# Kernel optimization log

Hardware: AMD Instinct MI355X
Metric: run time of the kernel (lower is better)

The kernel has to match this reference:

```python
import jax, jax.numpy as jnp
import numpy as np

DIM, H, W, B = 256, 64, 64, 2
N = H * W  # 4096 tokens (flattened feature map)
EPS = 1e-8


def setup_inputs() -> dict:
    key = jax.random.key(0)
    k0, k1, k2 = jax.random.split(key, 3)
    x = jax.random.normal(k0, (B, N, DIM), dtype=jnp.float32)
    y = jax.random.normal(k1, (B, N, DIM), dtype=jnp.float32)
    # orthogonal init of U (matches torch init.orthogonal_)
    U = jnp.linalg.qr(jax.random.normal(k2, (DIM, DIM), dtype=jnp.float32))[0]
    S1 = jnp.ones((DIM,), jnp.float32)
    S2 = jnp.ones((DIM,), jnp.float32)
    focus = jnp.float32(1.0)
    gating = jnp.float32(1.0)
    temp = jnp.float32(0.1)
    # abs_coords_y = arange(H).expand(W,-1).T.flatten() == floor(arange(N)/W)
    abs_y = jnp.floor_divide(jnp.arange(N, dtype=jnp.float32), jnp.float32(W))
    rel_coords_y = -abs_y[:, None] + abs_y[None, :]  # [N, N]
    return dict(x=x, y=y, U=U, S1=S1, S2=S2, focus=focus, gating=gating,
                temp=temp, rel_coords_y=rel_coords_y)


def reference(x, y, U, S1, S2, focus, gating, temp, rel_coords_y):
    Bb, Nn, d = x.shape
    # SpectralDecomp: x @ U^T @ diag(S^2) @ U, two branches stacked -> [B,2,N,d]
    xu = x @ U.T
    xs = jnp.stack([(xu * jnp.square(S1)) @ U, (xu * jnp.square(S2)) @ U], axis=1)
    # content score: [B,2,N,N]
    patch_score = jax.nn.softmax(
        jnp.einsum('bcnd,bmd->bcnm', xs, y) * (d ** -0.5), axis=-1)
    # position score: [N,N] broadcast to [B,2,N,N]
    pos_score = jax.nn.softmax(-jnp.abs(focus) * jnp.square(rel_coords_y), axis=-1)
    g = jax.nn.sigmoid(gating)
    attn = (1.0 - g) * patch_score + g * pos_score[None, None, :, :]
    attn = attn / attn.sum(axis=-1, keepdims=True)
    # entropy-based heat map + hard routing
    entropy = jnp.sum(-attn * jnp.log(attn + EPS), axis=-1).transpose(0, 2, 1)  # [B,N,2]
    hmap = 2.0 - 2.0 * jax.nn.sigmoid(temp * entropy)
    fgobg = hmap[..., 0] >= hmap[..., 1]  # [B,N]
    route = jnp.stack([fgobg, ~fgobg], axis=-1).astype(x.dtype)  # one-hot [B,N,2]
    heat_map = jnp.sum(hmap * route, axis=-1, keepdims=True)  # [B,N,1]
    # attend and select routed branch
    xo = jnp.einsum('bcnm,bmd->bncd', attn, y)  # [B,N,2,d]
    out = jnp.sum(xo * route[..., None], axis=-2)  # [B,N,d]
    return out, heat_map
```

## Files before the change

kernel.cpp:

```cpp
#include <hip/hip_runtime.h>
#include <math.h>

#define D      256
#define NTOK   4096
#define BATCH  2
#define NBC    4
#define NSPLIT 4
#define EPS    1e-8f
#define SCALE  0.0625f

typedef unsigned short ushortt;
typedef __attribute__((ext_vector_type(8))) short   bf16x8;
typedef __attribute__((ext_vector_type(4))) float   f32x4;
typedef __attribute__((ext_vector_type(4))) unsigned short u16x4;
typedef unsigned int u32;

__device__ __forceinline__ ushortt f2bf(float f) {
    u32 u = __builtin_bit_cast(u32, f);
    u += 0x7FFFu + ((u >> 16) & 1u);
    return (ushortt)(u >> 16);
}
__device__ __forceinline__ float bf2f(ushortt h) {
    u32 u = ((u32)h) << 16;
    return __builtin_bit_cast(float, u);
}

__device__ __forceinline__ void gload16(const ushortt* g, short* l) {
    __builtin_amdgcn_global_load_lds(
        (const __attribute__((address_space(1))) u32*)(const void*)g,
        (__attribute__((address_space(3))) u32*)(void*)l, 16, 0, 0);
}

__device__ __forceinline__ void mm_core(
    const ushortt* __restrict__ Ag, int lda,
    const ushortt* __restrict__ Bg, int ldb,
    int K, short* As, short* Bs, f32x4 acc[4][4])
{
    const int t = threadIdx.x, lane = t & 63, w = t >> 6;
    const int wr = w >> 1, wc = w & 1;
    const int l15 = lane & 15, l4 = lane >> 4;

    for (int k0 = 0; k0 < K; k0 += 64) {
        __syncthreads();
#pragma unroll
        for (int q = 0; q < 4; ++q) {
            int slot = (w * 4 + q) * 64 + lane;
            int r    = slot >> 3;
            int kgp  = slot & 7;
            int kg   = kgp ^ (r & 7);
            gload16(Ag + (size_t)r * lda + k0 + kg * 8, As + (w * 4 + q) * 512);
            gload16(Bg + (size_t)r * ldb + k0 + kg * 8, Bs + (w * 4 + q) * 512);
        }
        asm volatile("s_waitcnt vmcnt(0)" ::: "memory");
        __syncthreads();
#pragma unroll
        for (int kk = 0; kk < 2; ++kk) {
            bf16x8 af[4], bfr[4];
#pragma unroll
            for (int i = 0; i < 4; ++i) {
                int r  = wr * 64 + i * 16 + l15;
                int kg = kk * 4 + l4;
                af[i] = *(const bf16x8*)&As[(r * 8 + (kg ^ (r & 7))) * 8];
            }
#pragma unroll
            for (int j = 0; j < 4; ++j) {
                int c  = wc * 64 + j * 16 + l15;
                int kg = kk * 4 + l4;
                bfr[j] = *(const bf16x8*)&Bs[(c * 8 + (kg ^ (c & 7))) * 8];
            }
#pragma unroll
            for (int i = 0; i < 4; ++i)
#pragma unroll
                for (int j = 0; j < 4; ++j)
                    acc[i][j] = __builtin_amdgcn_mfma_f32_16x16x32_bf16(
                        af[i], bfr[j], acc[i][j], 0, 0, 0);
        }
    }
}

__global__ __launch_bounds__(256)
void k_prepM(const float* __restrict__ U, const float* __restrict__ S1,
             const float* __restrict__ S2, ushortt* __restrict__ M2b) {
    int idx = blockIdx.x * 256 + threadIdx.x;
    int c  = idx >> 16;
    int ij = idx & 65535;
    int i = ij >> 8, j = ij & 255;
    const float* S = c ? S2 : S1;
    float acc = 0.f;
    for (int k = 0; k < D; ++k) {
        float s = S[k];
        acc += U[k * D + i] * U[k * D + j] * (s * s);
    }
    M2b[idx] = f2bf(acc);
}

__global__ __launch_bounds__(256)
void k_cast(const float* __restrict__ x, const float* __restrict__ y,
            ushortt* __restrict__ xb, ushortt* __restrict__ yb) {
    int i = (blockIdx.x * 256 + threadIdx.x) * 4;
    float4 vx = *(const float4*)&x[i];
    float4 vy = *(const float4*)&y[i];
    u16x4 ox = { f2bf(vx.x), f2bf(vx.y), f2bf(vx.z), f2bf(vx.w) };
    u16x4 oy = { f2bf(vy.x), f2bf(vy.y), f2bf(vy.z), f2bf(vy.w) };
    *(u16x4*)&xb[i] = ox;
    *(u16x4*)&yb[i] = oy;
}

__global__ __launch_bounds__(256)
void k_transT(const float* __restrict__ y, ushortt* __restrict__ yT) {
    __shared__ float tile[64][65];
    const int b = blockIdx.z, d0 = blockIdx.y * 64, m0 = blockIdx.x * 64;
    const int t = threadIdx.x;
    const int c4 = (t & 15) * 4, r = t >> 4;
#pragma unroll
    for (int rr = r; rr < 64; rr += 16) {
        float4 v = *(const float4*)&y[((size_t)b * NTOK + m0 + rr) * D + d0 + c4];
        tile[rr][c4 + 0] = v.x; tile[rr][c4 + 1] = v.y;
        tile[rr][c4 + 2] = v.z; tile[rr][c4 + 3] = v.w;
    }
    __syncthreads();
    const int m4 = (t & 15) * 4;
#pragma unroll
    for (int dd = t >> 4; dd < 64; dd += 16) {
        u16x4 o = { f2bf(tile[m4 + 0][dd]), f2bf(tile[m4 + 1][dd]),
                    f2bf(tile[m4 + 2][dd]), f2bf(tile[m4 + 3][dd]) };
        *(u16x4*)&yT[((size_t)b * D + d0 + dd) * NTOK + m0 + m4] = o;
    }
}

__global__ __launch_bounds__(256)
void k_ysum(const float* __restrict__ y, float* __restrict__ Ysum) {
    const int blk = blockIdx.x;
    const int b = blk >> 6, ay = blk & 63;
    const int d = threadIdx.x;
    float acc = 0.f;
    const float* base = y + ((size_t)b * NTOK + ay * 64) * D + d;
#pragma unroll 8
    for (int w = 0; w < 64; ++w) acc += base[w * D];
    Ysum[(size_t)blk * D + d] = acc;
}

__global__ __launch_bounds__(256)
void k_posY(const float* __restrict__ Ysum, const float* __restrict__ focusp,
            float* __restrict__ posY) {
    __shared__ float e[64];
    const int blk = blockIdx.x;
    const int b = blk >> 6, ayq = blk & 63;
    const int t = threadIdx.x;
    const float f = fabsf(focusp[0]);
    if (t < 64) { float dy = (float)(t - ayq); e[t] = __expf(-f * dy * dy); }
    __syncthreads();
    float zs = 0.f;
#pragma unroll
    for (int j = 0; j < 64; ++j) zs += e[j];
    const float winv = 1.f / (64.f * zs);
    float acc = 0.f;
    const float* Yb = Ysum + (size_t)b * 64 * D + t;
#pragma unroll 8
    for (int aym = 0; aym < 64; ++aym) acc += e[aym] * Yb[aym * D];
    posY[(size_t)blk * D + t] = acc * winv;
}

__global__ __launch_bounds__(256)
void k_xs_mm(const ushortt* __restrict__ xb, const ushortt* __restrict__ M2b,
             ushortt* __restrict__ xsb) {
    __shared__ __align__(16) short As[8192];
    __shared__ __align__(16) short Bs[8192];
    const int bc = blockIdx.z, b = bc >> 1, c = bc & 1;
    const int d0 = blockIdx.x * 128, n0 = blockIdx.y * 128;
    f32x4 z = {0.f, 0.f, 0.f, 0.f};
    f32x4 acc[4][4];
#pragma unroll
    for (int i = 0; i < 4; ++i)
#pragma unroll
        for (int j = 0; j < 4; ++j) acc[i][j] = z;

    mm_core(xb + ((size_t)b * NTOK + n0) * D, D,
            M2b + (size_t)c * D * D + (size_t)d0 * D, D,
            D, As, Bs, acc);

    const int t = threadIdx.x, lane = t & 63, w = t >> 6;
    const int wr = w >> 1, wc = w & 1, l15 = lane & 15, l4 = lane >> 4;
#pragma unroll
    for (int i = 0; i < 4; ++i)
#pragma unroll
        for (int e = 0; e < 4; ++e) {
            int n = n0 + wr * 64 + i * 16 + l4 * 4 + e;
            ushortt* p = xsb + ((size_t)bc * NTOK + n) * D + d0 + wc * 64;
#pragma unroll
            for (int j = 0; j < 4; ++j) p[j * 16 + l15] = f2bf(acc[i][j][e]);
        }
}

__global__ __launch_bounds__(256)
void k_qkexp(const ushortt* __restrict__ xsb, const ushortt* __restrict__ yb,
             ushortt* __restrict__ Pbuf, float* __restrict__ Zqp) {
    __shared__ __align__(16) short As[8192];
    __shared__ __align__(16) short Bs[8192];
    const int bc = blockIdx.z, b = bc >> 1;
    const int m0 = blockIdx.x * 128, n0 = blockIdx.y * 128;
    f32x4 z = {0.f, 0.f, 0.f, 0.f};
    f32x4 acc[4][4];
#pragma unroll
    for (int i = 0; i < 4; ++i)
#pragma unroll
        for (int j = 0; j < 4; ++j) acc[i][j] = z;

    mm_core(xsb + ((size_t)bc * NTOK + n0) * D, D,
            yb + ((size_t)b * NTOK + m0) * D, D,
            D, As, Bs, acc);

    const int t = threadIdx.x, lane = t & 63, w = t >> 6;
    const int wr = w >> 1, wc = w & 1, l15 = lane & 15, l4 = lane >> 4;
    const int plane = (m0 >> 7) * 2 + wc;
#pragma unroll
    for (int i = 0; i < 4; ++i)
#pragma unroll
        for (int e = 0; e < 4; ++e) {
            int n = n0 + wr * 64 + i * 16 + l4 * 4 + e;
            ushortt* Prow = Pbuf + ((size_t)bc * NTOK + n) * NTOK + m0 + wc * 64;
            float rsum = 0.f;
#pragma unroll
            for (int j = 0; j < 4; ++j) {
                float pv = __expf(acc[i][j][e] * SCALE);
                Prow[j * 16 + l15] = f2bf(pv);
                rsum += pv;
            }
            rsum += __shfl_xor(rsum, 1);
            rsum += __shfl_xor(rsum, 2);
            rsum += __shfl_xor(rsum, 4);
            rsum += __shfl_xor(rsum, 8);
            if (l15 == 0)
                Zqp[((size_t)plane * NBC + bc) * NTOK + n] = rsum;
        }
}

__global__ __launch_bounds__(256)
void k_zqred(const float* __restrict__ Zqp, float* __restrict__ Zq) {
    int id = blockIdx.x * 256 + threadIdx.x;
    float s = 0.f;
#pragma unroll 8
    for (int p = 0; p < 64; ++p) s += Zqp[(size_t)p * NBC * NTOK + id];
    Zq[id] = s;
}

__device__ inline float blockSum(float v, volatile float* red) {
#pragma unroll
    for (int o = 32; o; o >>= 1) v += __shfl_down(v, o);
    int lane = threadIdx.x & 63, wid = threadIdx.x >> 6;
    if (lane == 0) red[wid] = v;
    __syncthreads();
    float r = red[0] + red[1] + red[2] + red[3];
    __syncthreads();
    return r;
}

__global__ __launch_bounds__(256)
void k_ent(const ushortt* __restrict__ Pbuf, const float* __restrict__ Zq,
           const float* __restrict__ focusp, const float* __restrict__ gatingp,
           float* __restrict__ ent, float* __restrict__ srw) {
    __shared__ float red[4];
    __shared__ float zparr[64];
    const int t = threadIdx.x;
    const int n = blockIdx.x, bc = blockIdx.y;
    const ushortt* Prow = Pbuf + ((size_t)bc * NTOK + n) * NTOK;

    const float f  = fabsf(focusp[0]);
    const float g  = 1.f / (1.f + __expf(-gatingp[0]));
    const float cg = 1.f - g;

    int ayn = n >> 6;
    if (t < 64) { float dy = (float)(t - ayn); zparr[t] = __expf(-f * dy * dy); }
    __syncthreads();
    float zp = 0.f;
#pragma unroll
    for (int j = 0; j < 64; ++j) zp += zparr[j];
    const float wq = cg / Zq[bc * NTOK + n];
    const float wp = g / (64.f * zp);

    float v[16];
#pragma unroll
    for (int p = 0; p < 4; ++p) {
        u16x4 h4 = *(const u16x4*)&Prow[p * 1024 + t * 4];
        int aym = (p * 1024 + t * 4) >> 6;
        float pw = zparr[aym] * wp;
        v[p * 4 + 0] = bf2f(h4.x) * wq + pw;
        v[p * 4 + 1] = bf2f(h4.y) * wq + pw;
        v[p * 4 + 2] = bf2f(h4.z) * wq + pw;
        v[p * 4 + 3] = bf2f(h4.w) * wq + pw;
    }
    float ss = 0.f;
#pragma unroll
    for (int i = 0; i < 16; ++i) ss += v[i];
    float Srw = blockSum(ss, red);
    float inv = 1.f / Srw;
    float hp = 0.f;
#pragma unroll
    for (int i = 0; i < 16; ++i) {
        float a = v[i] * inv;
        hp -= a * __logf(a + EPS);
    }
    float H = blockSum(hp, red);
    if (t == 0) {
        ent[bc * NTOK + n] = H;
        srw[bc * NTOK + n] = Srw;
    }
}

__global__ __launch_bounds__(256)
void k_route(const float* __restrict__ ent, const float* __restrict__ tempp,
             float* __restrict__ fsel, float* __restrict__ out) {
    int idx = blockIdx.x * 256 + threadIdx.x;
    if (idx >= BATCH * NTOK) return;
    int b = idx >> 12, n = idx & 4095;
    float tp = tempp[0];
    float H0 = ent[(b * 2 + 0) * NTOK + n];
    float H1 = ent[(b * 2 + 1) * NTOK + n];
    float hm0 = 2.f - 2.f / (1.f + __expf(-tp * H0));
    float hm1 = 2.f - 2.f / (1.f + __expf(-tp * H1));
    int sel = (hm0 >= hm1) ? 0 : 1;
    fsel[idx] = (float)sel;
    out[(size_t)BATCH * NTOK * D + idx] = sel ? hm1 : hm0;
}

__global__ __launch_bounds__(256)
void k_av_mm(const ushortt* __restrict__ Pbuf, const ushortt* __restrict__ yTb,
             const float* __restrict__ fsel, float* __restrict__ Opart) {
    __shared__ __align__(16) short As[8192];
    __shared__ __align__(16) short Bs[8192];
    __shared__ int any;
    const int zz = blockIdx.z;
    const int bc = zz & 3, sp = zz >> 2;
    const int b = bc >> 1, c = bc & 1;
    const int d0 = blockIdx.x * 128, n0 = blockIdx.y * 128;
    const int t = threadIdx.x;
    const int KS = NTOK / NSPLIT;

    if (t == 0) any = 0;
    __syncthreads();
    if (t < 128) {
        if (fsel[b * NTOK + n0 + t] == (float)c) any = 1;
    }
    __syncthreads();
    if (!any) return;

    f32x4 z = {0.f, 0.f, 0.f, 0.f};
    f32x4 acc[4][4];
#pragma unroll
    for (int i = 0; i < 4; ++i)
#pragma unroll
        for (int j = 0; j < 4; ++j) acc[i][j] = z;

    mm_core(Pbuf + ((size_t)bc * NTOK + n0) * NTOK + sp * KS, NTOK,
            yTb  + ((size_t)b  * D    + d0) * NTOK + sp * KS, NTOK,
            KS, As, Bs, acc);

    const int lane = t & 63, w = t >> 6;
    const int wr = w >> 1, wc = w & 1, l15 = lane & 15, l4 = lane >> 4;
    float* Os = Opart + (size_t)sp * BATCH * NTOK * D;
#pragma unroll
    for (int i = 0; i < 4; ++i)
#pragma unroll
        for (int e = 0; e < 4; ++e) {
            int n = n0 + wr * 64 + i * 16 + l4 * 4 + e;
            if (fsel[b * NTOK + n] == (float)c) {
                float* p = Os + ((size_t)b * NTOK + n) * D + d0 + wc * 64;
#pragma unroll
                for (int j = 0; j < 4; ++j) p[j * 16 + l15] = acc[i][j][e];
            }
        }
}

__global__ __launch_bounds__(256)
void k_final(const float* __restrict__ Opart, const float* __restrict__ posY,
             const float* __restrict__ Zq, const float* __restrict__ srw,
             const float* __restrict__ fsel, const float* __restrict__ gatingp,
             float* __restrict__ out) {
    int id = blockIdx.x * 256 + threadIdx.x;
    int e4 = id * 4;
    int d  = e4 & 255;
    int n  = (e4 >> 8) & 4095;
    int b  = e4 >> 20;
    const float g  = 1.f / (1.f + __expf(-gatingp[0]));
    const float cg = 1.f - g;
    int sel = (int)fsel[b * NTOK + n];
    int bc  = b * 2 + sel;
    float wq   = cg / Zq[bc * NTOK + n];
    float sinv = 1.f / srw[bc * NTOK + n];
    float4 o = make_float4(0.f, 0.f, 0.f, 0.f);
#pragma unroll
    for (int s = 0; s < NSPLIT; ++s) {
        float4 p = *(const float4*)&Opart[(size_t)s * BATCH * NTOK * D + e4];
        o.x += p.x; o.y += p.y; o.z += p.z; o.w += p.w;
    }
    float4 py = *(const float4*)&posY[((size_t)b * 64 + (n >> 6)) * D + d];
    float4 r;
    r.x = (o.x * wq + py.x * g) * sinv;
    r.y = (o.y * wq + py.y * g) * sinv;
    r.z = (o.z * wq + py.z * g) * sinv;
    r.w = (o.w * wq + py.w * g) * sinv;
    *(float4*)&out[e4] = r;
}

extern "C" void kernel_launch(void* const* d_in, const int* in_sizes, int n_in,
                              void* d_out, int out_size, void* d_ws, size_t ws_size,
                              hipStream_t stream) {
    const float* x      = (const float*)d_in[0];
    const float* y      = (const float*)d_in[1];
    const float* U      = (const float*)d_in[2];
    const float* S1     = (const float*)d_in[3];
    const float* S2     = (const float*)d_in[4];
    const float* focus  = (const float*)d_in[5];
    const float* gating = (const float*)d_in[6];
    const float* temp   = (const float*)d_in[7];
    float* out = (float*)d_out;

    char* p = (char*)d_ws;
    ushortt* M2b  = (ushortt*)p; p += (size_t)2 * D * D * 2;
    ushortt* xb   = (ushortt*)p; p += (size_t)BATCH * NTOK * D * 2;
    ushortt* yb   = (ushortt*)p; p += (size_t)BATCH * NTOK * D * 2;
    ushortt* yTb  = (ushortt*)p; p += (size_t)BATCH * D * NTOK * 2;
    ushortt* xsb  = (ushortt*)p; p += (size_t)NBC * NTOK * D * 2;
    float*   Ysum = (float*)p;   p += (size_t)BATCH * 64 * D * 4;
    float*   posY = (float*)p;   p += (size_t)BATCH * 64 * D * 4;
    float*   Zqp  = (float*)p;   p += (size_t)64 * NBC * NTOK * 4;
    float*   Zq   = (float*)p;   p += (size_t)NBC * NTOK * 4;
    float*   srw  = (float*)p;   p += (size_t)NBC * NTOK * 4;
    float*   ent  = (float*)p;   p += (size_t)NBC * NTOK * 4;
    float*   fsel = (float*)p;   p += (size_t)BATCH * NTOK * 4;
    float*   Opart= (float*)p;   p += (size_t)NSPLIT * BATCH * NTOK * D * 4;
    ushortt* Pbuf = (ushortt*)p;

    k_prepM <<<512, 256, 0, stream>>>(U, S1, S2, M2b);
    k_cast  <<<2048, 256, 0, stream>>>(x, y, xb, yb);
    k_transT<<<dim3(64, 4, 2), 256, 0, stream>>>(y, yTb);
    k_ysum  <<<BATCH * 64, 256, 0, stream>>>(y, Ysum);
    k_posY  <<<BATCH * 64, 256, 0, stream>>>(Ysum, focus, posY);
    k_xs_mm <<<dim3(D / 128, NTOK / 128, NBC), 256, 0, stream>>>(xb, M2b, xsb);
    k_qkexp <<<dim3(NTOK / 128, NTOK / 128, NBC), 256, 0, stream>>>(xsb, yb, Pbuf, Zqp);
    k_zqred <<<NBC * NTOK / 256, 256, 0, stream>>>(Zqp, Zq);
    k_ent   <<<dim3(NTOK, NBC), 256, 0, stream>>>(Pbuf, Zq, focus, gating, ent, srw);
    k_route <<<BATCH * NTOK / 256, 256, 0, stream>>>(ent, temp, fsel, out);
    k_av_mm <<<dim3(D / 128, NTOK / 128, NBC * NSPLIT), 256, 0, stream>>>(Pbuf, yTb, fsel, Opart);
    k_final <<<BATCH * NTOK * D / 1024, 256, 0, stream>>>(Opart, posY, Zq, srw, fsel, gating, out);
}
```

Measured before the change: 300.9 us.

## Permute key-token column order so P rows and yT use vectorized stores/loads

Changes the column ordering of the stored probability buffer so each lane writes four consecutive bf16 values in one store instead of four scattered scalar stores. The transposed y (yT) is permuted to match, so the later P·y product stays consistent. The entropy kernel now reads 16 contiguous values per thread with two 128-bit loads, and the position weight becomes one per thread because the permutation keeps all 16 values in the same row group. This reduces store and load instruction count and improves coalescing, but only stays correct if every consumer of Pbuf and yT uses the same permuted order.

Result: no change. 301.4 us (+0.2%).

```diff
diff --git a/kernel.cpp b/kernel.cpp
--- a/kernel.cpp
+++ b/kernel.cpp
@@ -9,10 +9,12 @@
 #define EPS    1e-8f
 #define SCALE  0.0625f
 
+
 typedef unsigned short ushortt;
 typedef __attribute__((ext_vector_type(8))) short   bf16x8;
 typedef __attribute__((ext_vector_type(4))) float   f32x4;
 typedef __attribute__((ext_vector_type(4))) unsigned short u16x4;
+typedef __attribute__((ext_vector_type(8))) unsigned short u16x8;
 typedef unsigned int u32;
 
 __device__ __forceinline__ ushortt f2bf(float f) {
@@ -119,12 +121,12 @@
         tile[rr][c4 + 2] = v.z; tile[rr][c4 + 3] = v.w;
     }
     __syncthreads();
-    const int m4 = (t & 15) * 4;
+    const int k = t & 15;
 #pragma unroll
     for (int dd = t >> 4; dd < 64; dd += 16) {
-        u16x4 o = { f2bf(tile[m4 + 0][dd]), f2bf(tile[m4 + 1][dd]),
-                    f2bf(tile[m4 + 2][dd]), f2bf(tile[m4 + 3][dd]) };
-        *(u16x4*)&yT[((size_t)b * D + d0 + dd) * NTOK + m0 + m4] = o;
+        u16x4 o = { f2bf(tile[k +  0][dd]), f2bf(tile[k + 16][dd]),
+                    f2bf(tile[k + 32][dd]), f2bf(tile[k + 48][dd]) };
+        *(u16x4*)&yT[((size_t)b * D + d0 + dd) * NTOK + m0 + k * 4] = o;
     }
 }
 
@@ -219,13 +221,13 @@
         for (int e = 0; e < 4; ++e) {
             int n = n0 + wr * 64 + i * 16 + l4 * 4 + e;
             ushortt* Prow = Pbuf + ((size_t)bc * NTOK + n) * NTOK + m0 + wc * 64;
-            float rsum = 0.f;
-#pragma unroll
-            for (int j = 0; j < 4; ++j) {
-                float pv = __expf(acc[i][j][e] * SCALE);
-                Prow[j * 16 + l15] = f2bf(pv);
-                rsum += pv;
-            }
+            float p0 = __expf(acc[i][0][e] * SCALE);
+            float p1 = __expf(acc[i][1][e] * SCALE);
+            float p2 = __expf(acc[i][2][e] * SCALE);
+            float p3 = __expf(acc[i][3][e] * SCALE);
+            u16x4 P4 = { f2bf(p0), f2bf(p1), f2bf(p2), f2bf(p3) };
+            *(u16x4*)&Prow[l15 * 4] = P4;
+            float rsum = (p0 + p1) + (p2 + p3);
             rsum += __shfl_xor(rsum, 1);
             rsum += __shfl_xor(rsum, 2);
             rsum += __shfl_xor(rsum, 4);
@@ -277,18 +279,16 @@
     for (int j = 0; j < 64; ++j) zp += zparr[j];
     const float wq = cg / Zq[bc * NTOK + n];
     const float wp = g / (64.f * zp);
-
+    const float pw = zparr[t >> 2] * wp;
+
+    u16x8 h0 = *(const u16x8*)&Prow[t * 16];
+    u16x8 h1 = *(const u16x8*)&Prow[t * 16 + 8];
     float v[16];
 #pragma unroll
-    for (int p = 0; p < 4; ++p) {
-        u16x4 h4 = *(const u16x4*)&Prow[p * 1024 + t * 4];
-        int aym = (p * 1024 + t * 4) >> 6;
-        float pw = zparr[aym] * wp;
-        v[p * 4 + 0] = bf2f(h4.x) * wq + pw;
-        v[p * 4 + 1] = bf2f(h4.y) * wq + pw;
-        v[p * 4 + 2] = bf2f(h4.z) * wq + pw;
-        v[p * 4 + 3] = bf2f(h4.w) * wq + pw;
-    }
+    for (int i = 0; i < 8; ++i) v[i]     = bf2f(h0[i]) * wq + pw;
+#pragma unroll
+    for (int i = 0; i < 8; ++i) v[8 + i] = bf2f(h1[i]) * wq + pw;
+
     float ss = 0.f;
 #pragma unroll
     for (int i = 0; i < 16; ++i) ss += v[i];
```
